# Performance work log

Hardware: AMD Instinct MI355X
Metric: run time of the kernel (lower is better)

The kernel has to match this reference:

```python
import jax, jax.numpy as jnp
import numpy as np

B, TQ, TK, D, R, H = 4, 2048, 2048, 1024, 64, 512
TAU_BASE, ASTRO_DECAY = 1.0, 0.95


def setup_inputs() -> dict:
    key = jax.random.key(0)
    ks = jax.random.split(key, 20)
    xav = lambda k, din, dout: jax.random.uniform(k, (din, dout), jnp.float32, -1.0, 1.0) * np.sqrt(6.0 / (din + dout))
    inp = {
        'q_in': jax.random.normal(ks[0], (B, TQ, D), jnp.float32),
        'k_in': jax.random.normal(ks[1], (B, TK, D), jnp.float32),
        'v_in': jax.random.normal(ks[2], (B, TK, D), jnp.float32),
        'astrocyte_state': jnp.zeros((B,), jnp.float32),
        'Wq': xav(ks[3], D, D), 'bq': jnp.zeros((D,), jnp.float32),
        'Wk': xav(ks[4], D, D), 'bk': jnp.zeros((D,), jnp.float32),
        'Wv': xav(ks[5], D, D), 'bv': jnp.zeros((D,), jnp.float32),
        'Wo': xav(ks[6], D, D), 'bo': jnp.zeros((D,), jnp.float32),
        # orthonormal role rows (R <= D): QR of a random D x R matrix, rows = Q^T
        'role_matrix': jnp.linalg.qr(jax.random.normal(ks[7], (D, R), jnp.float32))[0].T,
        'Wr1': xav(ks[8], D, H), 'br1': jnp.zeros((H,), jnp.float32),
        'Wr2': xav(ks[9], H, R),
        'astro_scale': jnp.ones((1,), jnp.float32),
    }
    return inp


def _l2norm(x, axis=-1, eps=1e-12):
    return x / jnp.clip(jnp.linalg.norm(x, axis=axis, keepdims=True), eps)


def _bind_vectors(a, b):
    # holographic (circular-convolution) binding via FFT along feature dim
    n = a.shape[-1]
    return jnp.fft.irfft(jnp.fft.rfft(a, axis=-1) * jnp.fft.rfft(b, axis=-1), n=n, axis=-1)


def _compute_surprise(Q):
    # per-token surprise: RMS-normalized L2 magnitude of projected queries -> (B, T_q)
    return jnp.linalg.norm(Q, axis=-1) / np.sqrt(Q.shape[-1])


def reference(q_in, k_in, v_in, astrocyte_state, Wq, bq, Wk, bk, Wv, bv, Wo, bo,
              role_matrix, Wr1, br1, Wr2, astro_scale):
    Q = q_in @ Wq + bq                      # (B,TQ,D)
    K = k_in @ Wk + bk                      # (B,TK,D)
    V = v_in @ Wv + bv                      # (B,TK,D)

    role_mat_norm = _l2norm(role_matrix)    # (R,D)
    role_logits = jax.nn.relu(K @ Wr1 + br1) @ Wr2          # (B,TK,R)
    role_weights = jax.nn.softmax(role_logits, axis=-1)
    role_vecs = role_weights @ role_mat_norm                 # (B,TK,D)
    K_bound = _bind_vectors(K, role_vecs)                    # (B,TK,D)

    surprise = _compute_surprise(Q)                          # (B,TQ)
    mean_surprise = surprise.mean(axis=-1)                   # (B,)
    new_state = ASTRO_DECAY * astrocyte_state + (1.0 - ASTRO_DECAY) * mean_surprise
    tau_eff = TAU_BASE * jnp.clip(1.0 + astro_scale * new_state, 0.001)[:, None, None]

    q_n = _l2norm(Q)
    k_n = _l2norm(K_bound)
    cos_sim = jnp.einsum('bqd,bkd->bqk', q_n, k_n)           # (B,TQ,TK)
    x = (cos_sim + 1.0) * 0.5
    scores = jnp.clip(1.0 - tau_eff * (1.0 - x) ** 2, 0.0)   # Epanechnikov kernel
    attn = scores / jnp.clip(scores.sum(axis=-1, keepdims=True), 1e-9)
    context = jnp.einsum('bqk,bkd->bqd', attn, V)
    output = context @ Wo + bo
    return output, new_state
```

## Files before the change

### kernel.cpp

```cpp
#include <hip/hip_runtime.h>
#include <stdint.h>


#define Bq 4
#define Tq 2048
#define Dd 1024
#define NT 8192
#define Hh 512
#define Rr_ 64
#define FQ 1024

typedef unsigned short ushort_t;
typedef short s16x8 __attribute__((ext_vector_type(8)));
typedef float floatx4 __attribute__((ext_vector_type(4)));

__device__ __forceinline__ float b2f(ushort_t s) {
  unsigned u = (unsigned)s << 16;
  return __builtin_bit_cast(float, u);
}
__device__ __forceinline__ ushort_t f2b(float f) {
  unsigned u = __builtin_bit_cast(unsigned, f);
  unsigned r = (u + 0x7fffu + ((u >> 16) & 1u)) >> 16;
  return (ushort_t)r;
}

__device__ __forceinline__ void load_lds16(const void* g, void* l) {
  __builtin_amdgcn_global_load_lds((__attribute__((address_space(1))) void*)(g),
                                   (__attribute__((address_space(3))) void*)(l),
                                   16, 0, 0);
}

__global__ __launch_bounds__(256) void gemm_bt(
    const ushort_t* __restrict__ A, const ushort_t* __restrict__ Bt,
    float* __restrict__ C, ushort_t* __restrict__ Cbf,
    const float* __restrict__ bias_col, const float* __restrict__ bias_row,
    const float* __restrict__ rmul, int rmulStride,
    const float* __restrict__ cmul, int cmulStride,
    const float* __restrict__ tau,
    float* __restrict__ rowsum, int rsStride, int rsMode,
    int K, int lda, int ldb, int ldc,
    long long sA, long long sB, long long sC, int flags)
{
  __shared__ __align__(16) ushort_t As[128 * 32];
  __shared__ __align__(16) ushort_t Bs[128 * 32];

  const int bz   = blockIdx.z;
  const ushort_t* Ab = A + (size_t)bz * sA;
  const ushort_t* Bb = Bt + (size_t)bz * sB;
  const int tm   = blockIdx.y * 128;
  const int tn   = blockIdx.x * 128;
  const int tid  = threadIdx.x;
  const int wave = tid >> 6;
  const int lane = tid & 63;
  const int wm   = (wave & 1) << 6;
  const int wn   = (wave >> 1) << 6;
  const int sr   = lane >> 2;
  const int cp   = lane & 3;
  const int sc   = (((cp - (sr >> 1)) & 3) << 3);
  const int fr   = lane & 15;
  const int fk   = ((((lane >> 4) + (fr >> 1)) & 3) << 3);

  floatx4 acc[4][4] = {};

  for (int k0 = 0; k0 < K; k0 += 32) {
    {
      const ushort_t* gA0 = Ab + (size_t)(tm + wave * 16 + sr) * lda + (k0 + sc);
      const ushort_t* gA1 = gA0 + (size_t)64 * lda;
      char* lA = (char*)As + wave * 1024;
      load_lds16(gA0, lA);
      load_lds16(gA1, lA + 4096);
      const ushort_t* gB0 = Bb + (size_t)(tn + wave * 16 + sr) * ldb + (k0 + sc);
      const ushort_t* gB1 = gB0 + (size_t)64 * ldb;
      char* lB = (char*)Bs + wave * 1024;
      load_lds16(gB0, lB);
      load_lds16(gB1, lB + 4096);
    }
    __syncthreads();
    s16x8 af[4], bfv[4];
#pragma unroll
    for (int i = 0; i < 4; i++)
      af[i] = *(const s16x8*)&As[(wm + i * 16 + fr) * 32 + fk];
#pragma unroll
    for (int j = 0; j < 4; j++)
      bfv[j] = *(const s16x8*)&Bs[(wn + j * 16 + fr) * 32 + fk];
#pragma unroll
    for (int i = 0; i < 4; i++)
#pragma unroll
      for (int j = 0; j < 4; j++)
        acc[i][j] = __builtin_amdgcn_mfma_f32_16x16x32_bf16(af[i], bfv[j], acc[i][j], 0, 0, 0);
    __syncthreads();
  }

  const float tv = tau ? tau[bz] : 0.f;
  float*   Cp  = C   ? C   + (size_t)bz * sC : nullptr;
  ushort_t* Cb = Cbf ? Cbf + (size_t)bz * sC : nullptr;
  float bcv[4], cmv[4];
#pragma unroll
  for (int j = 0; j < 4; j++) {
    const int col = tn + wn + j * 16 + (lane & 15);
    bcv[j] = bias_col ? bias_col[col] : 0.f;
    cmv[j] = cmul ? cmul[(size_t)bz * cmulStride + col] : 1.f;
  }
#pragma unroll
  for (int i = 0; i < 4; i++) {
#pragma unroll
    for (int r = 0; r < 4; r++) {
      const int row = tm + wm + i * 16 + (lane >> 4) * 4 + r;
      const float rm = rmul ? rmul[(size_t)bz * rmulStride + row] : 1.f;
      const float br = bias_row ? bias_row[row] : 0.f;
      float rsum = 0.f;
#pragma unroll
      for (int j = 0; j < 4; j++) {
        const int col = tn + wn + j * 16 + (lane & 15);
        float v = acc[i][j][r] + bcv[j] + br;
        v *= rm * cmv[j];
        if (flags & 1) v = fmaxf(v, 0.f);
        if (tau) { float d = 1.0f - v; v = fmaxf(1.0f - tv * 0.25f * d * d, 0.f); }
        rsum += (rsMode == 2) ? v * v : v;
        if (Cp) Cp[(size_t)row * ldc + col] = v;
        if (Cb) Cb[(size_t)row * ldc + col] = f2b(v);
      }
      if (rsMode == 1 || rsMode == 2) {
        rsum += __shfl_xor(rsum, 1);
        rsum += __shfl_xor(rsum, 2);
        rsum += __shfl_xor(rsum, 4);
        rsum += __shfl_xor(rsum, 8);
        if ((lane & 15) == 0)
          atomicAdd(&rowsum[(size_t)bz * rsStride + row], rsum);
      }
    }
  }
}

__global__ __launch_bounds__(256) void castbf(const float* __restrict__ in,
                                              ushort_t* __restrict__ out, int n4) {
  int i = blockIdx.x * 256 + threadIdx.x;
  if (i >= n4) return;
  float4 v = ((const float4*)in)[i];
  ushort4 o;
  o.x = f2b(v.x); o.y = f2b(v.y); o.z = f2b(v.z); o.w = f2b(v.w);
  ((ushort4*)out)[i] = o;
}

struct TC4 { const float* in[4]; ushort_t* out[4]; };
__global__ __launch_bounds__(256) void tcast4(TC4 p) {
  __shared__ float t[32][33];
  int z = blockIdx.z;
  const float* in = p.in[z];
  ushort_t* out = p.out[z];
  int r0 = blockIdx.x * 32, c0 = blockIdx.y * 32;
  int x = threadIdx.x, y = threadIdx.y;
  for (int dy = 0; dy < 32; dy += 8)
    t[y + dy][x] = in[(size_t)(r0 + y + dy) * 1024 + c0 + x];
  __syncthreads();
  for (int dy = 0; dy < 32; dy += 8)
    out[(size_t)(c0 + y + dy) * 1024 + r0 + x] = f2b(t[x][y + dy]);
}

__global__ __launch_bounds__(256) void tcast(const float* __restrict__ in,
                                             ushort_t* __restrict__ out,
                                             int RrN, int Cc, int Cp) {
  __shared__ float t[32][33];
  int r0 = blockIdx.x * 32, c0 = blockIdx.y * 32;
  int x = threadIdx.x, y = threadIdx.y;
  for (int dy = 0; dy < 32; dy += 8) {
    int r = r0 + y + dy, c = c0 + x;
    t[y + dy][x] = (c < Cc) ? in[(size_t)r * Cc + c] : 0.f;
  }
  __syncthreads();
  for (int dy = 0; dy < 32; dy += 8) {
    int c = c0 + y + dy, r = r0 + x;
    if (c < Cp) out[(size_t)c * RrN + r] = f2b(t[x][y + dy]);
  }
}

__global__ __launch_bounds__(256) void rolenorm(const float* __restrict__ rm,
                                                ushort_t* __restrict__ rmn) {
  int r = blockIdx.x, tid = threadIdx.x;
  float4 v = ((const float4*)(rm + (size_t)r * 1024))[tid];
  float s = v.x * v.x + v.y * v.y + v.z * v.z + v.w * v.w;
#pragma unroll
  for (int m = 1; m < 64; m <<= 1) s += __shfl_xor(s, m);
  __shared__ float red[6];
  if ((tid & 63) == 0) red[tid >> 6] = s;
  __syncthreads();
  if (tid == 0) red[4] = 1.f / fmaxf(sqrtf(red[0] + red[1] + red[2] + red[3]), 1e-12f);
  __syncthreads();
  float inv = red[4];
  ushort4 o;
  o.x = f2b(v.x * inv); o.y = f2b(v.y * inv); o.z = f2b(v.z * inv); o.w = f2b(v.w * inv);
  ((ushort4*)(rmn + (size_t)r * 1024))[tid] = o;
}

__global__ __launch_bounds__(256) void rfn_kernel(const ushort_t* __restrict__ rmn,
                                                  const ushort_t* __restrict__ ftab,
                                                  ushort_t* __restrict__ RFnT) {
  int f = blockIdx.x;
  int t = threadIdx.x;
  int r = t >> 2, part = t & 3;
  const ushort_t* fr = ftab + (size_t)f * 1024 + part * 256;
  const ushort_t* rr = rmn + (size_t)r * 1024 + part * 256;
  float s = 0.f;
#pragma unroll 4
  for (int i = 0; i < 32; i++) {
    s16x8 a = *(const s16x8*)(fr + i * 8);
    s16x8 b = *(const s16x8*)(rr + i * 8);
#pragma unroll
    for (int j = 0; j < 8; j++) s += b2f((ushort_t)a[j]) * b2f((ushort_t)b[j]);
  }
  s += __shfl_xor(s, 1);
  s += __shfl_xor(s, 2);
  if (part == 0) RFnT[(size_t)f * 128 + r] = f2b(s);
}

__global__ __launch_bounds__(256) void invnorm_surprise(const float* __restrict__ ssq,
                                                        float* __restrict__ invn,
                                                        float* __restrict__ ssum) {
  int row = blockIdx.x * 256 + threadIdx.x;
  float nrm = sqrtf(ssq[row]);
  invn[row] = 1.f / fmaxf(nrm, 1e-12f);
  float t = nrm;
#pragma unroll
  for (int m = 1; m < 64; m <<= 1) t += __shfl_xor(t, m);
  if ((threadIdx.x & 63) == 0) atomicAdd(&ssum[row >> 11], t);
}

__global__ __launch_bounds__(256) void invnorm(const float* __restrict__ ssq,
                                               float* __restrict__ invn) {
  int row = blockIdx.x * 256 + threadIdx.x;
  invn[row] = 1.f / fmaxf(sqrtf(ssq[row]), 1e-12f);
}

__global__ __launch_bounds__(256) void invrowsum(const float* __restrict__ rs,
                                                 float* __restrict__ inv) {
  int row = blockIdx.x * 256 + threadIdx.x;
  inv[row] = 1.f / fmaxf(rs[row], 1e-9f);
}

__global__ void finalize_astro(const float* __restrict__ ssum, const float* __restrict__ astro,
                               const float* __restrict__ ascale, float* __restrict__ tau,
                               float* __restrict__ outTail) {
  int b = threadIdx.x;
  if (b < Bq) {
    float mean = ssum[b] * (1.f / (32.f * 2048.f));
    float ns = 0.95f * astro[b] + 0.05f * mean;
    tau[b] = fmaxf(1.f + ascale[0] * ns, 0.001f);
    outTail[b] = ns;
  }
}

__global__ __launch_bounds__(256) void softmax64(const float* __restrict__ logits,
                                                 ushort_t* __restrict__ out) {
  int row = blockIdx.x * 4 + (threadIdx.x >> 6);
  int lane = threadIdx.x & 63;
  float x = logits[(size_t)row * 128 + lane];
  float m = x;
#pragma unroll
  for (int s = 1; s < 64; s <<= 1) m = fmaxf(m, __shfl_xor(m, s));
  float e = expf(x - m);
  float sum = e;
#pragma unroll
  for (int s = 1; s < 64; s <<= 1) sum += __shfl_xor(sum, s);
  out[(size_t)row * 64 + lane] = f2b(e / sum);
}

__global__ __launch_bounds__(256) void gen_ftab(ushort_t* __restrict__ ftab) {
  const float TW = 6.283185307179586f / 1024.f;
  int idx = blockIdx.x * 256 + threadIdx.x;
  int j = idx >> 10, k = idx & 1023;
  int f = j <= 512 ? j : j - 512;
  float th = (float)((f * k) & 1023) * TW;
  float sv, cv; sincosf(th, &sv, &cv);
  ftab[idx] = f2b(j <= 512 ? cv : -sv);
}
__global__ __launch_bounds__(256) void gen_itab(ushort_t* __restrict__ itab) {
  const float TW = 6.283185307179586f / 1024.f;
  int idx = blockIdx.x * 256 + threadIdx.x;
  int n = idx >> 10, j = idx & 1023;
  float v;
  if (j <= 512) {
    float w = (j == 0 || j == 512) ? (1.f / 1024.f) : (2.f / 1024.f);
    float th = (float)((j * n) & 1023) * TW;
    float sv, cv; sincosf(th, &sv, &cv);
    v = w * cv;
  } else {
    int f = j - 512;
    float th = (float)((f * n) & 1023) * TW;
    float sv, cv; sincosf(th, &sv, &cv);
    v = -(2.f / 1024.f) * sv;
  }
  itab[idx] = f2b(v);
}

__global__ __launch_bounds__(256) void fftmul(const ushort_t* __restrict__ KF,
                                              const ushort_t* __restrict__ RF,
                                              ushort_t* __restrict__ P) {
  int idx = blockIdx.x * 256 + threadIdx.x;
  int t = idx >> 9;
  int j = idx & 511;
  size_t base = (size_t)t * FQ;
  if (j == 0) {
    P[base]       = f2b(b2f(KF[base]) * b2f(RF[base]));
    P[base + 512] = f2b(b2f(KF[base + 512]) * b2f(RF[base + 512]));
  } else {
    float a = b2f(KF[base + j]), b = b2f(KF[base + 512 + j]);
    float c = b2f(RF[base + j]), d = b2f(RF[base + 512 + j]);
    P[base + j]       = f2b(a * c - b * d);
    P[base + 512 + j] = f2b(a * d + b * c);
  }
}

static constexpr size_t OFF_RS    = 0;
static constexpr size_t OFF_SSQQ  = 32768;
static constexpr size_t OFF_SSQK  = 65536;
static constexpr size_t OFF_INVQ  = 98304;
static constexpr size_t OFF_INVK  = 131072;
static constexpr size_t OFF_INVRS = 163840;
static constexpr size_t OFF_SSUM  = 196608;
static constexpr size_t OFF_TAU   = 196864;
static constexpr size_t OFF_WQT   = 197120;
static constexpr size_t OFF_WKT   = OFF_WQT  + 2097152;
static constexpr size_t OFF_WVT   = OFF_WKT  + 2097152;
static constexpr size_t OFF_WOT   = OFF_WVT  + 2097152;
static constexpr size_t OFF_WR1T  = OFF_WOT  + 2097152;
static constexpr size_t OFF_WR2T  = OFF_WR1T + 1048576;
static constexpr size_t OFF_RMN   = OFF_WR2T + 131072;
static constexpr size_t OFF_FTAB  = OFF_RMN  + 131072;
static constexpr size_t OFF_ITAB  = OFF_FTAB + 2097152;
static constexpr size_t OFF_RFNT  = OFF_ITAB + 2097152;
static constexpr size_t OFF_B1    = OFF_RFNT + 262144;
static constexpr size_t OFF_B2    = OFF_B1   + 16777216;
static constexpr size_t OFF_B3    = OFF_B2   + 16777216;
static constexpr size_t OFF_B4    = OFF_B3   + 16777216;
static constexpr size_t OFF_B5    = OFF_B4   + 16777216;
static constexpr size_t OFF_B6    = OFF_B5   + 16777216;
static constexpr size_t OFF_B7    = OFF_B6   + 16777216;
static constexpr size_t OFF_HID   = OFF_B7   + 16777216;
static constexpr size_t OFF_LOGI  = OFF_HID  + 8388608;
static constexpr size_t OFF_RW    = OFF_LOGI + 4194304;
static constexpr size_t OFF_SB    = OFF_RW   + 1048576;
static constexpr size_t WS_NEEDED = OFF_SB   + 33554432;

static inline void launch_gemm(hipStream_t s, const ushort_t* A, const ushort_t* Bt,
                               float* Cf, ushort_t* Cb,
                               const float* bias_col, const float* bias_row,
                               const float* rmul, int rmulStride,
                               const float* cmul, int cmulStride,
                               const float* tau, float* rowsum, int rsStride, int rsMode,
                               int M, int N, int K, int lda, int ldb, int ldc,
                               long long sA, long long sB, long long sC, int Z, int flags) {
  dim3 g(N / 128, M / 128, Z), b(256);
  gemm_bt<<<g, b, 0, s>>>(A, Bt, Cf, Cb, bias_col, bias_row, rmul, rmulStride,
                          cmul, cmulStride, tau, rowsum, rsStride, rsMode,
                          K, lda, ldb, ldc, sA, sB, sC, flags);
}

extern "C" void kernel_launch(void* const* d_in, const int* in_sizes, int n_in,
                              void* d_out, int out_size, void* d_ws, size_t ws_size,
                              hipStream_t stream) {
  (void)in_sizes; (void)n_in; (void)out_size;
  if (ws_size < WS_NEEDED) return;

  const float* q_in  = (const float*)d_in[0];
  const float* k_in  = (const float*)d_in[1];
  const float* v_in  = (const float*)d_in[2];
  const float* astro = (const float*)d_in[3];
  const float* Wq    = (const float*)d_in[4];
  const float* bq    = (const float*)d_in[5];
  const float* Wk    = (const float*)d_in[6];
  const float* bk    = (const float*)d_in[7];
  const float* Wv    = (const float*)d_in[8];
  const float* bv    = (const float*)d_in[9];
  const float* Wo    = (const float*)d_in[10];
  const float* bo    = (const float*)d_in[11];
  const float* roleM = (const float*)d_in[12];
  const float* Wr1   = (const float*)d_in[13];
  const float* br1   = (const float*)d_in[14];
  const float* Wr2   = (const float*)d_in[15];
  const float* ascl  = (const float*)d_in[16];

  char* ws = (char*)d_ws;
  float*    rowsumS = (float*)(ws + OFF_RS);
  float*    ssqQ    = (float*)(ws + OFF_SSQQ);
  float*    ssqK    = (float*)(ws + OFF_SSQK);
  float*    invQ    = (float*)(ws + OFF_INVQ);
  float*    invK    = (float*)(ws + OFF_INVK);
  float*    invRS   = (float*)(ws + OFF_INVRS);
  float*    ssum    = (float*)(ws + OFF_SSUM);
  float*    tau     = (float*)(ws + OFF_TAU);
  ushort_t* WqT  = (ushort_t*)(ws + OFF_WQT);
  ushort_t* WkT  = (ushort_t*)(ws + OFF_WKT);
  ushort_t* WvT  = (ushort_t*)(ws + OFF_WVT);
  ushort_t* WoT  = (ushort_t*)(ws + OFF_WOT);
  ushort_t* Wr1T = (ushort_t*)(ws + OFF_WR1T);
  ushort_t* Wr2T = (ushort_t*)(ws + OFF_WR2T);
  ushort_t* rmn  = (ushort_t*)(ws + OFF_RMN);
  ushort_t* FTab = (ushort_t*)(ws + OFF_FTAB);
  ushort_t* ITab = (ushort_t*)(ws + OFF_ITAB);
  ushort_t* RFnT = (ushort_t*)(ws + OFF_RFNT);
  ushort_t* qbf  = (ushort_t*)(ws + OFF_B1);
  ushort_t* KF   = (ushort_t*)(ws + OFF_B1);
  ushort_t* kinb = (ushort_t*)(ws + OFF_B2);
  ushort_t* RF   = (ushort_t*)(ws + OFF_B2);
  ushort_t* vinb = (ushort_t*)(ws + OFF_B3);
  ushort_t* Pb   = (ushort_t*)(ws + OFF_B3);
  ushort_t* qraw = (ushort_t*)(ws + OFF_B4);
  ushort_t* kbraw= (ushort_t*)(ws + OFF_B5);
  ushort_t* kp   = (ushort_t*)(ws + OFF_B6);
  ushort_t* ctx  = (ushort_t*)(ws + OFF_B6);
  ushort_t* vT   = (ushort_t*)(ws + OFF_B7);
  ushort_t* hid  = (ushort_t*)(ws + OFF_HID);
  float*    logi = (float*)(ws + OFF_LOGI);
  ushort_t* rw   = (ushort_t*)(ws + OFF_RW);
  ushort_t* Sb   = (ushort_t*)(ws + OFF_SB);
  float*    out  = (float*)d_out;

  hipMemsetAsync(ws, 0, OFF_SSUM + 256, stream);

  TC4 tc4;
  tc4.in[0] = Wq; tc4.in[1] = Wk; tc4.in[2] = Wv; tc4.in[3] = Wo;
  tc4.out[0] = WqT; tc4.out[1] = WkT; tc4.out[2] = WvT; tc4.out[3] = WoT;
  tcast4<<<dim3(32, 32, 4), dim3(32, 8), 0, stream>>>(tc4);
  tcast<<<dim3(32, 16), dim3(32, 8), 0, stream>>>(Wr1, Wr1T, 1024, 512, 512);
  tcast<<<dim3(16, 4),  dim3(32, 8), 0, stream>>>(Wr2, Wr2T, 512, 64, 128);
  rolenorm<<<64, 256, 0, stream>>>(roleM, rmn);
  gen_ftab<<<(FQ * 1024) / 256, 256, 0, stream>>>(FTab);
  gen_itab<<<(1024 * FQ) / 256, 256, 0, stream>>>(ITab);
  rfn_kernel<<<FQ, 256, 0, stream>>>(rmn, FTab, RFnT);

  castbf<<<8192, 256, 0, stream>>>(q_in, qbf, NT * Dd / 4);
  launch_gemm(stream, qbf, WqT, nullptr, qraw, bq, nullptr,
              nullptr, 0, nullptr, 0, nullptr, ssqQ, 0, 2,
              NT, Dd, Dd, Dd, Dd, Dd, 0, 0, 0, 1, 0);
  invnorm_surprise<<<NT / 256, 256, 0, stream>>>(ssqQ, invQ, ssum);
  finalize_astro<<<1, 64, 0, stream>>>(ssum, astro, ascl, tau, out + (size_t)NT * Dd);

  castbf<<<8192, 256, 0, stream>>>(k_in, kinb, NT * Dd / 4);
  launch_gemm(stream, kinb, WkT, nullptr, kp, bk, nullptr,
              nullptr, 0, nullptr, 0, nullptr, nullptr, 0, 0,
              NT, Dd, Dd, Dd, Dd, Dd, 0, 0, 0, 1, 0);

  castbf<<<8192, 256, 0, stream>>>(v_in, vinb, NT * Dd / 4);
  launch_gemm(stream, WvT, vinb, nullptr, vT, nullptr, bv,
              nullptr, 0, nullptr, 0, nullptr, nullptr, 0, 0,
              Dd, NT, Dd, Dd, Dd, NT, 0, 0, 0, 1, 0);

  launch_gemm(stream, kp, Wr1T, nullptr, hid, br1, nullptr,
              nullptr, 0, nullptr, 0, nullptr, nullptr, 0, 0,
              NT, Hh, Dd, Dd, Dd, Hh, 0, 0, 0, 1, 1 );
  launch_gemm(stream, hid, Wr2T, logi, nullptr, nullptr, nullptr,
              nullptr, 0, nullptr, 0, nullptr, nullptr, 0, 0,
              NT, 128, Hh, Hh, Hh, 128, 0, 0, 0, 1, 0);
  softmax64<<<NT / 4, 256, 0, stream>>>(logi, rw);

  launch_gemm(stream, kp, FTab, nullptr, KF, nullptr, nullptr,
              nullptr, 0, nullptr, 0, nullptr, nullptr, 0, 0,
              NT, FQ, Dd, Dd, Dd, FQ, 0, 0, 0, 1, 0);
  launch_gemm(stream, rw, RFnT, nullptr, RF, nullptr, nullptr,
              nullptr, 0, nullptr, 0, nullptr, nullptr, 0, 0,
              NT, FQ, Rr_, Rr_, 128, FQ, 0, 0, 0, 1, 0);
  fftmul<<<(NT * 512) / 256, 256, 0, stream>>>(KF, RF, Pb);
  launch_gemm(stream, Pb, ITab, nullptr, kbraw, nullptr, nullptr,
              nullptr, 0, nullptr, 0, nullptr, ssqK, 0, 2,
              NT, Dd, FQ, FQ, FQ, Dd, 0, 0, 0, 1, 0);
  invnorm<<<NT / 256, 256, 0, stream>>>(ssqK, invK);

  launch_gemm(stream, qraw, kbraw, nullptr, Sb, nullptr, nullptr,
              invQ, Tq, invK, Tq, tau, rowsumS, Tq, 1,
              Tq, Tq, Dd, Dd, Dd, Tq,
              (long long)Tq * Dd, (long long)Tq * Dd, (long long)Tq * Tq, Bq, 0);
  invrowsum<<<NT / 256, 256, 0, stream>>>(rowsumS, invRS);
  launch_gemm(stream, Sb, vT, nullptr, ctx, nullptr, nullptr,
              invRS, Tq, nullptr, 0, nullptr, nullptr, 0, 0,
              Tq, Dd, Tq, Tq, NT, Dd,
              (long long)Tq * Tq, (long long)Tq, (long long)Tq * Dd, Bq, 0);

  launch_gemm(stream, ctx, WoT, out, nullptr, bo, nullptr,
              nullptr, 0, nullptr, 0, nullptr, nullptr, 0, 0,
              NT, Dd, Dd, Dd, Dd, Dd, 0, 0, 0, 1, 0);
}
```

Baseline: 677.0 us.

## Fold Wo into V projection, widen GEMM K-tile, merge casts

The output projection is folded into the value projection: Wv·Wo is precomputed as a small 1024² GEMM and bv·Wo as a bias vector. This removes the final NT×D×D GEMM and the ctx round trip, and the attention GEMM now writes straight to the output with the bias added after row scaling. The shared GEMM kernel now stages a 64-wide K tile with a new 8-way LDS swizzle, halving the barrier count per K step. The three input casts and the Wv cast are merged into one multi-pointer launch. The cost is a small extra GEMM plus bias kernel, and an extra bf16 rounding of the fused weight.

```diff
diff --git a/kernel.cpp b/kernel.cpp
--- a/kernel.cpp
+++ b/kernel.cpp
@@ -41,8 +41,8 @@
     int K, int lda, int ldb, int ldc,
     long long sA, long long sB, long long sC, int flags)
 {
-  __shared__ __align__(16) ushort_t As[128 * 32];
-  __shared__ __align__(16) ushort_t Bs[128 * 32];
+  __shared__ __align__(16) ushort_t As[128 * 64];
+  __shared__ __align__(16) ushort_t Bs[128 * 64];
 
   const int bz   = blockIdx.z;
   const ushort_t* Ab = A + (size_t)bz * sA;
@@ -54,40 +54,55 @@
   const int lane = tid & 63;
   const int wm   = (wave & 1) << 6;
   const int wn   = (wave >> 1) << 6;
-  const int sr   = lane >> 2;
-  const int cp   = lane & 3;
-  const int sc   = (((cp - (sr >> 1)) & 3) << 3);
-  const int fr   = lane & 15;
-  const int fk   = ((((lane >> 4) + (fr >> 1)) & 3) << 3);
+  const int srow = lane >> 3;
+  const int sc   = (((lane & 7) - srow) & 7) << 3;
+  const int fr = lane & 15;
+  const int g  = lane >> 4;
+  const int c0 = (((g     + (fr & 7)) & 7) << 3);
+  const int c1 = (((g + 4 + (fr & 7)) & 7) << 3);
 
   floatx4 acc[4][4] = {};
 
-  for (int k0 = 0; k0 < K; k0 += 32) {
-    {
-      const ushort_t* gA0 = Ab + (size_t)(tm + wave * 16 + sr) * lda + (k0 + sc);
-      const ushort_t* gA1 = gA0 + (size_t)64 * lda;
-      char* lA = (char*)As + wave * 1024;
-      load_lds16(gA0, lA);
-      load_lds16(gA1, lA + 4096);
-      const ushort_t* gB0 = Bb + (size_t)(tn + wave * 16 + sr) * ldb + (k0 + sc);
-      const ushort_t* gB1 = gB0 + (size_t)64 * ldb;
-      char* lB = (char*)Bs + wave * 1024;
-      load_lds16(gB0, lB);
-      load_lds16(gB1, lB + 4096);
+  const ushort_t* gA = Ab + (size_t)(tm + wave * 32 + srow) * lda + sc;
+  const ushort_t* gB = Bb + (size_t)(tn + wave * 32 + srow) * ldb + sc;
+  char* lA = (char*)As + wave * 4096;
+  char* lB = (char*)Bs + wave * 4096;
+
+  for (int k0 = 0; k0 < K; k0 += 64) {
+#pragma unroll
+    for (int q = 0; q < 4; q++) {
+      load_lds16(gA + (size_t)(q * 8) * lda + k0, lA + q * 1024);
+      load_lds16(gB + (size_t)(q * 8) * ldb + k0, lB + q * 1024);
     }
     __syncthreads();
-    s16x8 af[4], bfv[4];
-#pragma unroll
-    for (int i = 0; i < 4; i++)
-      af[i] = *(const s16x8*)&As[(wm + i * 16 + fr) * 32 + fk];
-#pragma unroll
-    for (int j = 0; j < 4; j++)
-      bfv[j] = *(const s16x8*)&Bs[(wn + j * 16 + fr) * 32 + fk];
-#pragma unroll
-    for (int i = 0; i < 4; i++)
+    {
+      s16x8 af[4], bfv[4];
+#pragma unroll
+      for (int i = 0; i < 4; i++)
+        af[i] = *(const s16x8*)&As[(wm + i * 16 + fr) * 64 + c0];
 #pragma unroll
       for (int j = 0; j < 4; j++)
-        acc[i][j] = __builtin_amdgcn_mfma_f32_16x16x32_bf16(af[i], bfv[j], acc[i][j], 0, 0, 0);
+        bfv[j] = *(const s16x8*)&Bs[(wn + j * 16 + fr) * 64 + c0];
+#pragma unroll
+      for (int i = 0; i < 4; i++)
+#pragma unroll
+        for (int j = 0; j < 4; j++)
+          acc[i][j] = __builtin_amdgcn_mfma_f32_16x16x32_bf16(af[i], bfv[j], acc[i][j], 0, 0, 0);
+    }
+    {
+      s16x8 af[4], bfv[4];
+#pragma unroll
+      for (int i = 0; i < 4; i++)
+        af[i] = *(const s16x8*)&As[(wm + i * 16 + fr) * 64 + c1];
+#pragma unroll
+      for (int j = 0; j < 4; j++)
+        bfv[j] = *(const s16x8*)&Bs[(wn + j * 16 + fr) * 64 + c1];
+#pragma unroll
+      for (int i = 0; i < 4; i++)
+#pragma unroll
+        for (int j = 0; j < 4; j++)
+          acc[i][j] = __builtin_amdgcn_mfma_f32_16x16x32_bf16(af[i], bfv[j], acc[i][j], 0, 0, 0);
+    }
     __syncthreads();
   }
 
@@ -112,8 +127,9 @@
 #pragma unroll
       for (int j = 0; j < 4; j++) {
         const int col = tn + wn + j * 16 + (lane & 15);
-        float v = acc[i][j][r] + bcv[j] + br;
-        v *= rm * cmv[j];
+        float v;
+        if (flags & 2) v = acc[i][j][r] * rm * cmv[j] + bcv[j] + br;
+        else           v = (acc[i][j][r] + bcv[j] + br) * rm * cmv[j];
         if (flags & 1) v = fmaxf(v, 0.f);
         if (tau) { float d = 1.0f - v; v = fmaxf(1.0f - tv * 0.25f * d * d, 0.f); }
         rsum += (rsMode == 2) ? v * v : v;
@@ -132,18 +148,19 @@
   }
 }
 
-__global__ __launch_bounds__(256) void castbf(const float* __restrict__ in,
-                                              ushort_t* __restrict__ out, int n4) {
+struct CastM { const float* in[4]; ushort_t* out[4]; int n4[4]; };
+__global__ __launch_bounds__(256) void castM_kernel(CastM p) {
+  int z = blockIdx.z;
   int i = blockIdx.x * 256 + threadIdx.x;
-  if (i >= n4) return;
-  float4 v = ((const float4*)in)[i];
+  if (i >= p.n4[z]) return;
+  float4 v = ((const float4*)p.in[z])[i];
   ushort4 o;
   o.x = f2b(v.x); o.y = f2b(v.y); o.z = f2b(v.z); o.w = f2b(v.w);
-  ((ushort4*)out)[i] = o;
-}
-
-struct TC4 { const float* in[4]; ushort_t* out[4]; };
-__global__ __launch_bounds__(256) void tcast4(TC4 p) {
+  ((ushort4*)p.out[z])[i] = o;
+}
+
+struct TC3 { const float* in[3]; ushort_t* out[3]; };
+__global__ __launch_bounds__(256) void tcast3(TC3 p) {
   __shared__ float t[32][33];
   int z = blockIdx.z;
   const float* in = p.in[z];
@@ -211,6 +228,20 @@
   s += __shfl_xor(s, 1);
   s += __shfl_xor(s, 2);
   if (part == 0) RFnT[(size_t)f * 128 + r] = f2b(s);
+}
+
+__global__ __launch_bounds__(256) void bvo_kernel(const ushort_t* __restrict__ WoT,
+                                                  const float* __restrict__ bv,
+                                                  float* __restrict__ bvo) {
+  int d = blockIdx.x * 4 + (threadIdx.x >> 6);
+  int lane = threadIdx.x & 63;
+  const ushort_t* row = WoT + (size_t)d * 1024;
+  float s = 0.f;
+#pragma unroll
+  for (int i = 0; i < 16; i++) s += b2f(row[lane + 64 * i]) * bv[lane + 64 * i];
+#pragma unroll
+  for (int m = 1; m < 64; m <<= 1) s += __shfl_xor(s, m);
+  if (lane == 0) bvo[d] = s;
 }
 
 __global__ __launch_bounds__(256) void invnorm_surprise(const float* __restrict__ ssq,
@@ -318,11 +349,13 @@
 static constexpr size_t OFF_INVRS = 163840;
 static constexpr size_t OFF_SSUM  = 196608;
 static constexpr size_t OFF_TAU   = 196864;
-static constexpr size_t OFF_WQT   = 197120;
+static constexpr size_t OFF_BVO   = 197120;
+static constexpr size_t OFF_WQT   = 201216;
 static constexpr size_t OFF_WKT   = OFF_WQT  + 2097152;
-static constexpr size_t OFF_WVT   = OFF_WKT  + 2097152;
-static constexpr size_t OFF_WOT   = OFF_WVT  + 2097152;
-static constexpr size_t OFF_WR1T  = OFF_WOT  + 2097152;
+static constexpr size_t OFF_WOT   = OFF_WKT  + 2097152;
+static constexpr size_t OFF_WVBF  = OFF_WOT  + 2097152;
+static constexpr size_t OFF_WVOT  = OFF_WVBF + 2097152;
+static constexpr size_t OFF_WR1T  = OFF_WVOT + 2097152;
 static constexpr size_t OFF_WR2T  = OFF_WR1T + 1048576;
 static constexpr size_t OFF_RMN   = OFF_WR2T + 131072;
 static constexpr size_t OFF_FTAB  = OFF_RMN  + 131072;
@@ -388,10 +421,12 @@
   float*    invRS   = (float*)(ws + OFF_INVRS);
   float*    ssum    = (float*)(ws + OFF_SSUM);
   float*    tau     = (float*)(ws + OFF_TAU);
+  float*    bvo     = (float*)(ws + OFF_BVO);
   ushort_t* WqT  = (ushort_t*)(ws + OFF_WQT);
   ushort_t* WkT  = (ushort_t*)(ws + OFF_WKT);
-  ushort_t* WvT  = (ushort_t*)(ws + OFF_WVT);
   ushort_t* WoT  = (ushort_t*)(ws + OFF_WOT);
+  ushort_t* Wvbf = (ushort_t*)(ws + OFF_WVBF);
+  ushort_t* WvoT = (ushort_t*)(ws + OFF_WVOT);
   ushort_t* Wr1T = (ushort_t*)(ws + OFF_WR1T);
   ushort_t* Wr2T = (ushort_t*)(ws + OFF_WR2T);
   ushort_t* rmn  = (ushort_t*)(ws + OFF_RMN);
@@ -407,20 +442,19 @@
   ushort_t* qraw = (ushort_t*)(ws + OFF_B4);
   ushort_t* kbraw= (ushort_t*)(ws + OFF_B5);
   ushort_t* kp   = (ushort_t*)(ws + OFF_B6);
-  ushort_t* ctx  = (ushort_t*)(ws + OFF_B6);
-  ushort_t* vT   = (ushort_t*)(ws + OFF_B7);
+  ushort_t* VoT  = (ushort_t*)(ws + OFF_B7);
   ushort_t* hid  = (ushort_t*)(ws + OFF_HID);
   float*    logi = (float*)(ws + OFF_LOGI);
   ushort_t* rw   = (ushort_t*)(ws + OFF_RW);
   ushort_t* Sb   = (ushort_t*)(ws + OFF_SB);
   float*    out  = (float*)d_out;
 
-  hipMemsetAsync(ws, 0, OFF_SSUM + 256, stream);
-
-  TC4 tc4;
-  tc4.in[0] = Wq; tc4.in[1] = Wk; tc4.in[2] = Wv; tc4.in[3] = Wo;
-  tc4.out[0] = WqT; tc4.out[1] = WkT; tc4.out[2] = WvT; tc4.out[3] = WoT;
-  tcast4<<<dim3(32, 32, 4), dim3(32, 8), 0, stream>>>(tc4);
+  hipMemsetAsync(ws, 0, OFF_BVO, stream);
+
+  TC3 tc3;
+  tc3.in[0] = Wq; tc3.in[1] = Wk; tc3.in[2] = Wo;
+  tc3.out[0] = WqT; tc3.out[1] = WkT; tc3.out[2] = WoT;
+  tcast3<<<dim3(32, 32, 3), dim3(32, 8), 0, stream>>>(tc3);
   tcast<<<dim3(32, 16), dim3(32, 8), 0, stream>>>(Wr1, Wr1T, 1024, 512, 512);
   tcast<<<dim3(16, 4),  dim3(32, 8), 0, stream>>>(Wr2, Wr2T, 512, 64, 128);
   rolenorm<<<64, 256, 0, stream>>>(roleM, rmn);
@@ -428,20 +462,29 @@
   gen_itab<<<(1024 * FQ) / 256, 256, 0, stream>>>(ITab);
   rfn_kernel<<<FQ, 256, 0, stream>>>(rmn, FTab, RFnT);
 
-  castbf<<<8192, 256, 0, stream>>>(q_in, qbf, NT * Dd / 4);
+  CastM cm;
+  cm.in[0] = q_in; cm.out[0] = qbf;  cm.n4[0] = NT * Dd / 4;
+  cm.in[1] = k_in; cm.out[1] = kinb; cm.n4[1] = NT * Dd / 4;
+  cm.in[2] = v_in; cm.out[2] = vinb; cm.n4[2] = NT * Dd / 4;
+  cm.in[3] = Wv;   cm.out[3] = Wvbf; cm.n4[3] = Dd * Dd / 4;
+  castM_kernel<<<dim3(8192, 1, 4), 256, 0, stream>>>(cm);
+
+  bvo_kernel<<<256, 256, 0, stream>>>(WoT, bv, bvo);
+  launch_gemm(stream, WoT, Wvbf, nullptr, WvoT, nullptr, nullptr,
+              nullptr, 0, nullptr, 0, nullptr, nullptr, 0, 0,
+              Dd, Dd, Dd, Dd, Dd, Dd, 0, 0, 0, 1, 0);
+
   launch_gemm(stream, qbf, WqT, nullptr, qraw, bq, nullptr,
               nullptr, 0, nullptr, 0, nullptr, ssqQ, 0, 2,
               NT, Dd, Dd, Dd, Dd, Dd, 0, 0, 0, 1, 0);
   invnorm_surprise<<<NT / 256, 256, 0, stream>>>(ssqQ, invQ, ssum);
   finalize_astro<<<1, 64, 0, stream>>>(ssum, astro, ascl, tau, out + (size_t)NT * Dd);
 
-  castbf<<<8192, 256, 0, stream>>>(k_in, kinb, NT * Dd / 4);
   launch_gemm(stream, kinb, WkT, nullptr, kp, bk, nullptr,
               nullptr, 0, nullptr, 0, nullptr, nullptr, 0, 0,
               NT, Dd, Dd, Dd, Dd, Dd, 0, 0, 0, 1, 0);
 
-  castbf<<<8192, 256, 0, stream>>>(v_in, vinb, NT * Dd / 4);
-  launch_gemm(stream, WvT, vinb, nullptr, vT, nullptr, bv,
+  launch_gemm(stream, WvoT, vinb, nullptr, VoT, nullptr, bvo,
               nullptr, 0, nullptr, 0, nullptr, nullptr, 0, 0,
               Dd, NT, Dd, Dd, Dd, NT, 0, 0, 0, 1, 0);
 
@@ -470,12 +513,8 @@
               Tq, Tq, Dd, Dd, Dd, Tq,
               (long long)Tq * Dd, (long long)Tq * Dd, (long long)Tq * Tq, Bq, 0);
   invrowsum<<<NT / 256, 256, 0, stream>>>(rowsumS, invRS);
-  launch_gemm(stream, Sb, vT, nullptr, ctx, nullptr, nullptr,
+  launch_gemm(stream, Sb, VoT, out, nullptr, bo, nullptr,
               invRS, Tq, nullptr, 0, nullptr, nullptr, 0, 0,
               Tq, Dd, Tq, Tq, NT, Dd,
-              (long long)Tq * Tq, (long long)Tq, (long long)Tq * Dd, Bq, 0);
-
-  launch_gemm(stream, ctx, WoT, out, nullptr, bo, nullptr,
-              nullptr, 0, nullptr, 0, nullptr, nullptr, 0, 0,
-              NT, Dd, Dd, Dd, Dd, Dd, 0, 0, 0, 1, 0);
-}
+              (long long)Tq * Tq, (long long)Tq, (long long)Tq * Dd, Bq, 2 );
+}
```

New measurement: 684.3 us. Within noise of the previous version (+1.1%).
